# Kernel tuning notes

Measured on AMD Instinct MI355X. Metric: run time of the kernel, lower is better.

The kernel has to match this reference:

```python
import jax, jax.numpy as jnp
import numpy as np

# Model dims (see init_kwargs)
N_SITES = 1024
M_CAT = 2
TOKEN_DIM = 256
POS_DIM = 768
D_MODEL = TOKEN_DIM + POS_DIM  # 1024
D_FF = 4 * D_MODEL             # 4096
N_LAYERS = 4
N_HEADS = 16
HEAD_DIM = D_MODEL // N_HEADS  # 64
BATCH = 4
EPS = 1e-5


def setup_inputs() -> dict:
    key = jax.random.key(0)
    ks = jax.random.split(key, 8)
    s = 0.02  # init std, matches _init_weights
    L = N_LAYERS
    return {
        "x": jax.random.randint(ks[0], (BATCH, N_SITES), 0, M_CAT),
        "tok_emb": jax.random.normal(ks[1], (M_CAT, TOKEN_DIM), jnp.float32) * s,
        "pos_emb": jax.random.normal(ks[2], (N_SITES, POS_DIM), jnp.float32) * s,
        "w_qkv": jax.random.normal(ks[3], (L, 3 * D_MODEL, D_MODEL), jnp.float32) * s,
        "b_qkv": jnp.zeros((L, 3 * D_MODEL), jnp.float32),
        "ln1_g": jnp.ones((L, D_MODEL), jnp.float32),
        "ln1_b": jnp.zeros((L, D_MODEL), jnp.float32),
        "ln2_g": jnp.ones((L, D_MODEL), jnp.float32),
        "ln2_b": jnp.zeros((L, D_MODEL), jnp.float32),
        "ff_w1": jax.random.normal(ks[4], (L, D_FF, D_MODEL), jnp.float32) * s,
        "ff_b1": jnp.zeros((L, D_FF), jnp.float32),
        "ff_w2": jax.random.normal(ks[5], (L, D_MODEL, D_FF), jnp.float32) * s,
        "ff_b2": jnp.zeros((L, D_MODEL), jnp.float32),
        "out_w": jax.random.normal(ks[6], (M_CAT, D_MODEL), jnp.float32) * s,
        "out_b": jnp.zeros((M_CAT,), jnp.float32),
    }


def _layernorm(h, g, b):
    mu = jnp.mean(h, axis=-1, keepdims=True)
    var = jnp.mean(jnp.square(h - mu), axis=-1, keepdims=True)
    return (h - mu) * jax.lax.rsqrt(var + EPS) * g + b


def _forward(x, tok_emb, pos_emb, w_qkv, b_qkv, ln1_g, ln1_b, ln2_g, ln2_b,
             ff_w1, ff_b1, ff_w2, ff_b2, out_w, out_b):
    B, T = x.shape
    # shift right: prepend BOS token '1', drop last
    x_in = jnp.concatenate([jnp.ones((B, 1), dtype=x.dtype), x[:, :-1]], axis=1)
    h = jnp.concatenate([
        tok_emb[x_in],                                       # [B, T, TOKEN_DIM]
        jnp.broadcast_to(pos_emb[None, :T], (B, T, POS_DIM)),
    ], axis=-1)                                              # [B, T, D_MODEL]
    causal = jnp.tril(jnp.ones((T, T), dtype=bool))
    scale = 1.0 / np.sqrt(HEAD_DIM)
    for l in range(N_LAYERS):
        a = _layernorm(h, ln1_g[l], ln1_b[l])
        qkv = a @ w_qkv[l].T + b_qkv[l]                      # [B, T, 3*D]
        q, k, v = jnp.split(qkv, 3, axis=-1)
        q = q.reshape(B, T, N_HEADS, HEAD_DIM)
        k = k.reshape(B, T, N_HEADS, HEAD_DIM)
        v = v.reshape(B, T, N_HEADS, HEAD_DIM)
        scores = jnp.einsum('bthd,bshd->bhts', q, k) * scale
        scores = jnp.where(causal, scores, jnp.float32(-1e9))
        p = jax.nn.softmax(scores, axis=-1)
        attn = jnp.einsum('bhts,bshd->bthd', p, v).reshape(B, T, D_MODEL)
        h = h + attn                                          # residual (no out_proj, per decode loop)
        h = _layernorm(h, ln2_g[l], ln2_b[l])
        ff = jax.nn.gelu(h @ ff_w1[l].T + ff_b1[l]) @ ff_w2[l].T + ff_b2[l]
        h = h + ff
    logits = h @ out_w.T + out_b                              # [B, T, M]
    return jax.nn.log_softmax(logits, axis=-1)


def reference(x, tok_emb, pos_emb, w_qkv, b_qkv, ln1_g, ln1_b, ln2_g, ln2_b,
              ff_w1, ff_b1, ff_w2, ff_b2, out_w, out_b):
    return _forward(x, tok_emb, pos_emb, w_qkv, b_qkv, ln1_g, ln1_b, ln2_g, ln2_b,
                    ff_w1, ff_b1, ff_w2, ff_b2, out_w, out_b)
```

## Files before the change

### kernel.cpp

```cpp
#include <hip/hip_runtime.h>
#include <cstddef>
#include <cstdint>

#define BB   4
#define TS   1024
#define DM   1024
#define DFF  4096
#define NHD  16
#define HDM  64
#define NLY  4
#define TOKD 256
#define POSD 768

typedef __bf16 bf16_t;
typedef __bf16 bf16x4 __attribute__((ext_vector_type(4)));
typedef __bf16 bf16x8 __attribute__((ext_vector_type(8)));
typedef float  f32x4  __attribute__((ext_vector_type(4)));

#define GLOAD_LDS16(gp, lp)                                                  \
  __builtin_amdgcn_global_load_lds(                                          \
      (const __attribute__((address_space(1))) void*)(gp),                   \
      (__attribute__((address_space(3))) void*)(lp), 16, 0, 0)

__device__ __forceinline__ float gelu_f(float x) {
  float x3 = x * x * x;
  return 0.5f * x * (1.0f + tanhf(0.7978845608028654f * (x + 0.044715f * x3)));
}

__global__ __launch_bounds__(256) void k_embed(const int* __restrict__ x,
    const float* __restrict__ tok, const float* __restrict__ pos,
    bf16_t* __restrict__ h) {
  int idx = (blockIdx.x * 256 + threadIdx.x) * 4;
  int d  = idx & (DM - 1);
  int bt = idx >> 10;
  int t  = bt & (TS - 1);
  int b  = bt >> 10;
  float4 v;
  if (d < TOKD) {
    int tk = (t == 0) ? 1 : x[b * TS + t - 1];
    v = *(const float4*)(tok + tk * TOKD + d);
  } else {
    v = *(const float4*)(pos + (size_t)t * POSD + (d - TOKD));
  }
  bf16x4 o = { (bf16_t)v.x, (bf16_t)v.y, (bf16_t)v.z, (bf16_t)v.w };
  *(bf16x4*)(h + idx) = o;
}

__global__ __launch_bounds__(256) void k_ln(const bf16_t* __restrict__ in,
    const float* __restrict__ g, const float* __restrict__ bta,
    bf16_t* __restrict__ out1, bf16_t* __restrict__ out2) {
  int row  = blockIdx.x * 4 + (threadIdx.x >> 6);
  int lane = threadIdx.x & 63;
  const bf16_t* p = in + (size_t)row * DM + lane * 16;
  bf16x8 v0 = *(const bf16x8*)p;
  bf16x8 v1 = *(const bf16x8*)(p + 8);
  float vals[16];
  float s = 0.f, s2 = 0.f;
#pragma unroll
  for (int i = 0; i < 8; i++) { vals[i] = (float)v0[i]; vals[8 + i] = (float)v1[i]; }
#pragma unroll
  for (int i = 0; i < 16; i++) { s += vals[i]; s2 += vals[i] * vals[i]; }
#pragma unroll
  for (int off = 32; off; off >>= 1) {
    s  += __shfl_xor(s, off);
    s2 += __shfl_xor(s2, off);
  }
  float mu  = s * (1.f / DM);
  float var = s2 * (1.f / DM) - mu * mu;
  float rs  = rsqrtf(var + 1e-5f);
  bf16x8 o0, o1;
#pragma unroll
  for (int i = 0; i < 16; i++) {
    int d = lane * 16 + i;
    float v = (vals[i] - mu) * rs * g[d] + bta[d];
    if (i < 8) o0[i] = (bf16_t)v; else o1[i - 8] = (bf16_t)v;
  }
  size_t off = (size_t)row * DM + lane * 16;
  if (out1) { *(bf16x8*)(out1 + off) = o0; *(bf16x8*)(out1 + off + 8) = o1; }
  if (out2) { *(bf16x8*)(out2 + off) = o0; *(bf16x8*)(out2 + off + 8) = o1; }
}

template <bool GELU, bool ACC>
__global__ __launch_bounds__(256) void k_gemm(
    const bf16_t* __restrict__ A, const float* __restrict__ B,
    const float* __restrict__ bias, bf16_t* __restrict__ C,
    int M, int N, int K, int ldb) {
  __shared__ __align__(16) bf16_t As[128 * 32];
  __shared__ __align__(16) bf16_t Bs[128 * 32];
  const int tid  = threadIdx.x;
  const int wave = tid >> 6, lane = tid & 63;
  const int m0 = blockIdx.y * 128, n0 = blockIdx.x * 128;
  const int wm = (wave >> 1) * 64, wn = (wave & 1) * 64;
  f32x4 acc[4][4];
#pragma unroll
  for (int i = 0; i < 4; i++)
#pragma unroll
    for (int j = 0; j < 4; j++) acc[i][j] = {0.f, 0.f, 0.f, 0.f};

  const int srow = wave * 16 + (lane >> 2);
  const int scol = (lane & 3) * 8;
  const bf16_t* Ag = A + (size_t)(m0 + srow) * K + scol;
  bf16_t* AsW = As + wave * 16 * 32;
  const int brow = tid >> 3;
  const int bcol = (tid & 7) * 4;
  const float* Bg = B + (size_t)(n0 + brow) * ldb + bcol;
  const int fr = lane & 15, fq = lane >> 4;

  for (int k0 = 0; k0 < K; k0 += 32) {
    __syncthreads();
    GLOAD_LDS16(Ag + k0, AsW);
    GLOAD_LDS16(Ag + (size_t)64 * K + k0, AsW + 64 * 32);
#pragma unroll
    for (int i = 0; i < 4; i++) {
      float4 v = *(const float4*)(Bg + (size_t)(i * 32) * ldb + k0);
      bf16x4 o = { (bf16_t)v.x, (bf16_t)v.y, (bf16_t)v.z, (bf16_t)v.w };
      *(bf16x4*)&Bs[(brow + i * 32) * 32 + bcol] = o;
    }
    __syncthreads();
    bf16x8 af[4], bfv[4];
#pragma unroll
    for (int i = 0; i < 4; i++)
      af[i] = *(const bf16x8*)&As[(wm + i * 16 + fr) * 32 + fq * 8];
#pragma unroll
    for (int j = 0; j < 4; j++)
      bfv[j] = *(const bf16x8*)&Bs[(wn + j * 16 + fr) * 32 + fq * 8];
#pragma unroll
    for (int i = 0; i < 4; i++)
#pragma unroll
      for (int j = 0; j < 4; j++)
        acc[i][j] = __builtin_amdgcn_mfma_f32_16x16x32_bf16(
            af[i], bfv[j], acc[i][j], 0, 0, 0);
  }
#pragma unroll
  for (int i = 0; i < 4; i++) {
#pragma unroll
    for (int j = 0; j < 4; j++) {
#pragma unroll
      for (int r = 0; r < 4; r++) {
        int m = m0 + wm + i * 16 + fq * 4 + r;
        int n = n0 + wn + j * 16 + fr;
        float v = acc[i][j][r];
        if (bias) v += bias[n];
        if (GELU) v = gelu_f(v);
        size_t off = (size_t)m * N + n;
        if (ACC) C[off] = (bf16_t)((float)C[off] + v);
        else     C[off] = (bf16_t)v;
      }
    }
  }
}

__global__ __launch_bounds__(256) void k_flash(const bf16_t* __restrict__ qkv,
                                               bf16_t* __restrict__ hres) {
  __shared__ __align__(16) bf16_t Qs[64 * 72];
  __shared__ __align__(16) bf16_t Ks[64 * 72];
  __shared__ __align__(16) bf16_t Vt[64 * 72];
  const int hh = blockIdx.x, qt = blockIdx.y, bz = blockIdx.z;
  const int tid = threadIdx.x;
  const int w = tid >> 6, lane = tid & 63;
  const int fr = lane & 15, fq = lane >> 4;
  const int sr = tid >> 2, seg = tid & 3;
  const bf16_t* base = qkv + (size_t)bz * TS * (3 * DM) + hh * HDM;
  bf16_t* Ps = Qs;

  {
    const bf16_t* qrow = base + (size_t)(qt * 64 + sr) * (3 * DM) + seg * 16;
    *(bf16x8*)&Qs[sr * 72 + seg * 16]     = *(const bf16x8*)qrow;
    *(bf16x8*)&Qs[sr * 72 + seg * 16 + 8] = *(const bf16x8*)(qrow + 8);
  }
  __syncthreads();
  bf16x8 aq[2];
  aq[0] = *(const bf16x8*)&Qs[(w * 16 + fr) * 72 + fq * 8];
  aq[1] = *(const bf16x8*)&Qs[(w * 16 + fr) * 72 + 32 + fq * 8];

  f32x4 o[4];
#pragma unroll
  for (int d = 0; d < 4; d++) o[d] = {0.f, 0.f, 0.f, 0.f};
  float mval[4] = {-1e30f, -1e30f, -1e30f, -1e30f};
  float lsum[4] = {0.f, 0.f, 0.f, 0.f};

  for (int st = 0; st <= qt; st++) {
    __syncthreads();
    {
      size_t rowoff = (size_t)(st * 64 + sr) * (3 * DM);
      const bf16_t* krow = base + rowoff + DM + seg * 16;
      *(bf16x8*)&Ks[sr * 72 + seg * 16]     = *(const bf16x8*)krow;
      *(bf16x8*)&Ks[sr * 72 + seg * 16 + 8] = *(const bf16x8*)(krow + 8);
      const bf16_t* vrow = base + rowoff + 2 * DM + seg * 16;
      bf16x8 v0 = *(const bf16x8*)vrow;
      bf16x8 v1 = *(const bf16x8*)(vrow + 8);
#pragma unroll
      for (int j = 0; j < 8; j++) Vt[(seg * 16 + j) * 72 + sr]     = v0[j];
#pragma unroll
      for (int j = 0; j < 8; j++) Vt[(seg * 16 + 8 + j) * 72 + sr] = v1[j];
    }
    __syncthreads();
    f32x4 sacc[4];
#pragma unroll
    for (int j = 0; j < 4; j++) sacc[j] = {0.f, 0.f, 0.f, 0.f};
#pragma unroll
    for (int j = 0; j < 4; j++)
#pragma unroll
      for (int hf = 0; hf < 2; hf++) {
        bf16x8 bk = *(const bf16x8*)&Ks[(j * 16 + fr) * 72 + hf * 32 + fq * 8];
        sacc[j] = __builtin_amdgcn_mfma_f32_16x16x32_bf16(aq[hf], bk, sacc[j],
                                                          0, 0, 0);
      }
#pragma unroll
    for (int j = 0; j < 4; j++)
#pragma unroll
      for (int r = 0; r < 4; r++) {
        float s = sacc[j][r] * 0.125f;
        if (st == qt && (j * 16 + fr) > (w * 16 + fq * 4 + r)) s = -1e30f;
        sacc[j][r] = s;
      }
    float corr[4];
#pragma unroll
    for (int r = 0; r < 4; r++) {
      float v = fmaxf(fmaxf(sacc[0][r], sacc[1][r]),
                      fmaxf(sacc[2][r], sacc[3][r]));
      v = fmaxf(v, __shfl_xor(v, 1));
      v = fmaxf(v, __shfl_xor(v, 2));
      v = fmaxf(v, __shfl_xor(v, 4));
      v = fmaxf(v, __shfl_xor(v, 8));
      float mn = fmaxf(mval[r], v);
      corr[r] = __expf(mval[r] - mn);
      mval[r] = mn;
      lsum[r] *= corr[r];
    }
#pragma unroll
    for (int d = 0; d < 4; d++)
#pragma unroll
      for (int r = 0; r < 4; r++) o[d][r] *= corr[r];
    float rsum[4] = {0.f, 0.f, 0.f, 0.f};
#pragma unroll
    for (int j = 0; j < 4; j++)
#pragma unroll
      for (int r = 0; r < 4; r++) {
        float p = __expf(sacc[j][r] - mval[r]);
        rsum[r] += p;
        Ps[(w * 16 + fq * 4 + r) * 72 + j * 16 + fr] = (bf16_t)p;
      }
#pragma unroll
    for (int r = 0; r < 4; r++) {
      float v = rsum[r];
      v += __shfl_xor(v, 1);
      v += __shfl_xor(v, 2);
      v += __shfl_xor(v, 4);
      v += __shfl_xor(v, 8);
      lsum[r] += v;
    }
    __syncthreads();
    bf16x8 ap[2];
    ap[0] = *(const bf16x8*)&Ps[(w * 16 + fr) * 72 + fq * 8];
    ap[1] = *(const bf16x8*)&Ps[(w * 16 + fr) * 72 + 32 + fq * 8];
#pragma unroll
    for (int d = 0; d < 4; d++)
#pragma unroll
      for (int hf = 0; hf < 2; hf++) {
        bf16x8 bv = *(const bf16x8*)&Vt[(d * 16 + fr) * 72 + hf * 32 + fq * 8];
        o[d] = __builtin_amdgcn_mfma_f32_16x16x32_bf16(ap[hf], bv, o[d],
                                                       0, 0, 0);
      }
  }
#pragma unroll
  for (int r = 0; r < 4; r++) {
    float inv = 1.0f / lsum[r];
    bf16_t* row = hres + (size_t)bz * TS * DM +
                  (size_t)(qt * 64 + w * 16 + fq * 4 + r) * DM + hh * HDM;
#pragma unroll
    for (int d = 0; d < 4; d++) {
      int c = d * 16 + fr;
      row[c] = (bf16_t)((float)row[c] + o[d][r] * inv);
    }
  }
}

__global__ __launch_bounds__(256) void k_logits(const bf16_t* __restrict__ h,
    const float* __restrict__ w, const float* __restrict__ bz,
    float* __restrict__ out) {
  int row  = blockIdx.x * 4 + (threadIdx.x >> 6);
  int lane = threadIdx.x & 63;
  const bf16_t* hp = h + (size_t)row * DM + lane * 16;
  bf16x8 a0 = *(const bf16x8*)hp;
  bf16x8 a1 = *(const bf16x8*)(hp + 8);
  float s0 = 0.f, s1 = 0.f;
#pragma unroll
  for (int i = 0; i < 16; i++) {
    float v = (float)(i < 8 ? a0[i] : a1[i - 8]);
    int d = lane * 16 + i;
    s0 += v * w[d];
    s1 += v * w[DM + d];
  }
#pragma unroll
  for (int off = 32; off; off >>= 1) {
    s0 += __shfl_xor(s0, off);
    s1 += __shfl_xor(s1, off);
  }
  if (lane == 0) {
    float z0 = s0 + bz[0], z1 = s1 + bz[1];
    float mx  = fmaxf(z0, z1);
    float lse = mx + logf(expf(z0 - mx) + expf(z1 - mx));
    out[row * 2]     = z0 - lse;
    out[row * 2 + 1] = z1 - lse;
  }
}

extern "C" void kernel_launch(void* const* d_in, const int* in_sizes, int n_in,
                              void* d_out, int out_size, void* d_ws, size_t ws_size,
                              hipStream_t stream) {
  const int*   x     = (const int*)d_in[0];
  const float* tokE  = (const float*)d_in[1];
  const float* posE  = (const float*)d_in[2];
  const float* w_qkv = (const float*)d_in[3];
  const float* b_qkv = (const float*)d_in[4];
  const float* ln1g  = (const float*)d_in[5];
  const float* ln1b  = (const float*)d_in[6];
  const float* ln2g  = (const float*)d_in[7];
  const float* ln2b  = (const float*)d_in[8];
  const float* fw1   = (const float*)d_in[9];
  const float* fb1   = (const float*)d_in[10];
  const float* fw2   = (const float*)d_in[11];
  const float* fb2   = (const float*)d_in[12];
  const float* outw  = (const float*)d_in[13];
  const float* outb  = (const float*)d_in[14];
  float* out = (float*)d_out;

  const size_t NT = (size_t)BB * TS;
  const size_t MB = 1024 * 1024;
  bf16_t* h_bf = (bf16_t*)d_ws;
  char*   S    = (char*)d_ws + 8 * MB;
  bf16_t* a_bf   = (bf16_t*)S;
  bf16_t* qkv_bf = (bf16_t*)(S + 4 * MB);
  bf16_t* a2_bf  = (bf16_t*)S;
  bf16_t* f1_bf  = (bf16_t*)(S + 8 * MB);

  k_embed<<<(NT * DM) / 1024, 256, 0, stream>>>(x, tokE, posE, h_bf);
  for (int l = 0; l < NLY; l++) {
    for (int g = 0; g < 2; g++) {
      bf16_t* hg = h_bf + (size_t)g * 2 * TS * DM;
      k_ln<<<2 * TS / 4, 256, 0, stream>>>(hg, ln1g + l * DM, ln1b + l * DM,
                                           a_bf, nullptr);
      k_gemm<false, false><<<dim3(3 * DM / 128, 2 * TS / 128), 256, 0, stream>>>(
          a_bf, w_qkv + (size_t)l * 3 * DM * DM, b_qkv + l * 3 * DM, qkv_bf,
          2 * TS, 3 * DM, DM, DM);
      k_flash<<<dim3(NHD, TS / 64, 2), 256, 0, stream>>>(qkv_bf, hg);
    }
    k_ln<<<NT / 4, 256, 0, stream>>>(h_bf, ln2g + l * DM, ln2b + l * DM,
                                     h_bf, a2_bf);
    for (int s = 0; s < 2; s++) {
      k_gemm<true, false><<<dim3(2048 / 128, NT / 128), 256, 0, stream>>>(
          a2_bf, fw1 + (size_t)l * DFF * DM + (size_t)s * 2048 * DM,
          fb1 + l * DFF + s * 2048, f1_bf, NT, 2048, DM, DM);
      k_gemm<false, true><<<dim3(DM / 128, NT / 128), 256, 0, stream>>>(
          f1_bf, fw2 + (size_t)l * DM * DFF + s * 2048,
          s == 0 ? fb2 + l * DM : nullptr, h_bf, NT, DM, 2048, DFF);
    }
  }
  k_logits<<<NT / 4, 256, 0, stream>>>(h_bf, outw, outb, out);
}
```

Measured before the change: 2.217 ms.

## Double-buffer GEMM LDS tiles to overlap global loads with MFMA compute

Splits the A and B shared-memory tiles into two ping-pong buffers. The next K-tile's global-to-LDS A loads and the B register loads are issued before the current tile's MFMAs run, and the converted B values are written to LDS afterwards. This cuts the loop to one barrier per iteration and hides load latency behind compute. In exchange it doubles LDS use, which may lower occupancy, and keeps extra B values live in registers.

```diff
diff --git a/kernel.cpp b/kernel.cpp
--- a/kernel.cpp
+++ b/kernel.cpp
@@ -85,8 +85,8 @@
     const bf16_t* __restrict__ A, const float* __restrict__ B,
     const float* __restrict__ bias, bf16_t* __restrict__ C,
     int M, int N, int K, int ldb) {
-  __shared__ __align__(16) bf16_t As[128 * 32];
-  __shared__ __align__(16) bf16_t Bs[128 * 32];
+  __shared__ __align__(16) bf16_t As[2][128 * 32];
+  __shared__ __align__(16) bf16_t Bs[2][128 * 32];
   const int tid  = threadIdx.x;
   const int wave = tid >> 6, lane = tid & 63;
   const int m0 = blockIdx.y * 128, n0 = blockIdx.x * 128;
@@ -100,36 +100,61 @@
   const int srow = wave * 16 + (lane >> 2);
   const int scol = (lane & 3) * 8;
   const bf16_t* Ag = A + (size_t)(m0 + srow) * K + scol;
-  bf16_t* AsW = As + wave * 16 * 32;
+  const int aw0 = wave * 16 * 32;
+  const int aw1 = (64 + wave * 16) * 32;
   const int brow = tid >> 3;
   const int bcol = (tid & 7) * 4;
   const float* Bg = B + (size_t)(n0 + brow) * ldb + bcol;
   const int fr = lane & 15, fq = lane >> 4;
-
-  for (int k0 = 0; k0 < K; k0 += 32) {
-    __syncthreads();
-    GLOAD_LDS16(Ag + k0, AsW);
-    GLOAD_LDS16(Ag + (size_t)64 * K + k0, AsW + 64 * 32);
-#pragma unroll
-    for (int i = 0; i < 4; i++) {
-      float4 v = *(const float4*)(Bg + (size_t)(i * 32) * ldb + k0);
-      bf16x4 o = { (bf16_t)v.x, (bf16_t)v.y, (bf16_t)v.z, (bf16_t)v.w };
-      *(bf16x4*)&Bs[(brow + i * 32) * 32 + bcol] = o;
-    }
-    __syncthreads();
+  const int nt = K >> 5;
+
+  float4 breg[4];
+  GLOAD_LDS16(Ag, &As[0][aw0]);
+  GLOAD_LDS16(Ag + (size_t)64 * K, &As[0][aw1]);
+#pragma unroll
+  for (int i = 0; i < 4; i++)
+    breg[i] = *(const float4*)(Bg + (size_t)(i * 32) * ldb);
+#pragma unroll
+  for (int i = 0; i < 4; i++) {
+    bf16x4 o = { (bf16_t)breg[i].x, (bf16_t)breg[i].y,
+                 (bf16_t)breg[i].z, (bf16_t)breg[i].w };
+    *(bf16x4*)&Bs[0][(brow + i * 32) * 32 + bcol] = o;
+  }
+  __syncthreads();
+
+  int p = 0;
+  for (int t = 0; t < nt; t++, p ^= 1) {
+    const bool more = (t + 1 < nt);
+    const int k1 = (t + 1) << 5;
+    if (more) {
+      GLOAD_LDS16(Ag + k1, &As[p ^ 1][aw0]);
+      GLOAD_LDS16(Ag + (size_t)64 * K + k1, &As[p ^ 1][aw1]);
+#pragma unroll
+      for (int i = 0; i < 4; i++)
+        breg[i] = *(const float4*)(Bg + (size_t)(i * 32) * ldb + k1);
+    }
     bf16x8 af[4], bfv[4];
 #pragma unroll
     for (int i = 0; i < 4; i++)
-      af[i] = *(const bf16x8*)&As[(wm + i * 16 + fr) * 32 + fq * 8];
+      af[i] = *(const bf16x8*)&As[p][(wm + i * 16 + fr) * 32 + fq * 8];
 #pragma unroll
     for (int j = 0; j < 4; j++)
-      bfv[j] = *(const bf16x8*)&Bs[(wn + j * 16 + fr) * 32 + fq * 8];
+      bfv[j] = *(const bf16x8*)&Bs[p][(wn + j * 16 + fr) * 32 + fq * 8];
 #pragma unroll
     for (int i = 0; i < 4; i++)
 #pragma unroll
       for (int j = 0; j < 4; j++)
         acc[i][j] = __builtin_amdgcn_mfma_f32_16x16x32_bf16(
             af[i], bfv[j], acc[i][j], 0, 0, 0);
+    if (more) {
+#pragma unroll
+      for (int i = 0; i < 4; i++) {
+        bf16x4 o = { (bf16_t)breg[i].x, (bf16_t)breg[i].y,
+                     (bf16_t)breg[i].z, (bf16_t)breg[i].w };
+        *(bf16x4*)&Bs[p ^ 1][(brow + i * 32) * 32 + bcol] = o;
+      }
+    }
+    __syncthreads();
   }
 #pragma unroll
   for (int i = 0; i < 4; i++) {
```

Measured after the change: 2.076 ms. 1.07x faster.

## Triple-buffer GEMM LDS with register-staged B prefetch and templated N tile

Applied to the files above, without the earlier changes.

The GEMM's main loop becomes a software pipeline with three LDS stages. A tiles are issued two steps ahead through global_load_lds, and B tiles are prefetched into registers and written to LDS one step later. A single barrier per k-step replaces the two, and explicit vmcnt/lgkmcnt waits let global loads overlap MFMA compute. The N tile width is now a template parameter, with 64 used for the QKV and FF2 GEMMs to double the number of blocks. The cost is more LDS and register use, which may lower occupancy.

```diff
diff --git a/kernel.cpp b/kernel.cpp
--- a/kernel.cpp
+++ b/kernel.cpp
@@ -80,61 +80,104 @@
   if (out2) { *(bf16x8*)(out2 + off) = o0; *(bf16x8*)(out2 + off + 8) = o1; }
 }
 
-template <bool GELU, bool ACC>
+template <bool GELU, bool ACC, int TN>
 __global__ __launch_bounds__(256) void k_gemm(
     const bf16_t* __restrict__ A, const float* __restrict__ B,
     const float* __restrict__ bias, bf16_t* __restrict__ C,
     int M, int N, int K, int ldb) {
-  __shared__ __align__(16) bf16_t As[128 * 32];
-  __shared__ __align__(16) bf16_t Bs[128 * 32];
+  constexpr int NJ   = TN / 32;
+  constexpr int GOPS = 2 + NJ;
+  __shared__ __align__(16) bf16_t As[3][128 * 32];
+  __shared__ __align__(16) bf16_t Bs[3][TN * 32];
   const int tid  = threadIdx.x;
   const int wave = tid >> 6, lane = tid & 63;
-  const int m0 = blockIdx.y * 128, n0 = blockIdx.x * 128;
-  const int wm = (wave >> 1) * 64, wn = (wave & 1) * 64;
-  f32x4 acc[4][4];
+  const int m0 = blockIdx.y * 128, n0 = blockIdx.x * TN;
+  const int wm = (wave >> 1) * 64, wn = (wave & 1) * (TN / 2);
+  f32x4 acc[4][NJ];
 #pragma unroll
   for (int i = 0; i < 4; i++)
 #pragma unroll
-    for (int j = 0; j < 4; j++) acc[i][j] = {0.f, 0.f, 0.f, 0.f};
+    for (int j = 0; j < NJ; j++) acc[i][j] = {0.f, 0.f, 0.f, 0.f};
 
   const int srow = wave * 16 + (lane >> 2);
   const int scol = (lane & 3) * 8;
   const bf16_t* Ag = A + (size_t)(m0 + srow) * K + scol;
-  bf16_t* AsW = As + wave * 16 * 32;
+  const int aw0 = wave * 16 * 32;
+  const int aw1 = (64 + wave * 16) * 32;
   const int brow = tid >> 3;
   const int bcol = (tid & 7) * 4;
   const float* Bg = B + (size_t)(n0 + brow) * ldb + bcol;
   const int fr = lane & 15, fq = lane >> 4;
-
-  for (int k0 = 0; k0 < K; k0 += 32) {
-    __syncthreads();
-    GLOAD_LDS16(Ag + k0, AsW);
-    GLOAD_LDS16(Ag + (size_t)64 * K + k0, AsW + 64 * 32);
-#pragma unroll
-    for (int i = 0; i < 4; i++) {
-      float4 v = *(const float4*)(Bg + (size_t)(i * 32) * ldb + k0);
-      bf16x4 o = { (bf16_t)v.x, (bf16_t)v.y, (bf16_t)v.z, (bf16_t)v.w };
-      *(bf16x4*)&Bs[(brow + i * 32) * 32 + bcol] = o;
-    }
-    __syncthreads();
-    bf16x8 af[4], bfv[4];
-#pragma unroll
-    for (int i = 0; i < 4; i++)
-      af[i] = *(const bf16x8*)&As[(wm + i * 16 + fr) * 32 + fq * 8];
-#pragma unroll
-    for (int j = 0; j < 4; j++)
-      bfv[j] = *(const bf16x8*)&Bs[(wn + j * 16 + fr) * 32 + fq * 8];
-#pragma unroll
-    for (int i = 0; i < 4; i++)
-#pragma unroll
-      for (int j = 0; j < 4; j++)
-        acc[i][j] = __builtin_amdgcn_mfma_f32_16x16x32_bf16(
-            af[i], bfv[j], acc[i][j], 0, 0, 0);
-  }
+  const int nt = K >> 5;
+
+  float4 br0[NJ], br1[NJ];
+
+#define ISSUE_A(g) do { const int _k = (g) << 5; const int _b = (g) % 3;     \
+    GLOAD_LDS16(Ag + _k, &As[_b][aw0]);                                      \
+    GLOAD_LDS16(Ag + (size_t)64 * K + _k, &As[_b][aw1]); } while (0)
+#define LOAD_B(g, br) do { const int _k = (g) << 5;                          \
+    _Pragma("unroll")                                                        \
+    for (int _i = 0; _i < NJ; _i++)                                          \
+      br[_i] = *(const float4*)(Bg + (size_t)(_i * 32) * ldb + _k); } while (0)
+#define WRITE_B(g, br) do { const int _b = (g) % 3;                          \
+    _Pragma("unroll")                                                        \
+    for (int _i = 0; _i < NJ; _i++) {                                        \
+      bf16x4 _o = { (bf16_t)br[_i].x, (bf16_t)br[_i].y,                      \
+                    (bf16_t)br[_i].z, (bf16_t)br[_i].w };                    \
+      *(bf16x4*)&Bs[_b][(brow + _i * 32) * 32 + bcol] = _o; } } while (0)
+#define COMPUTE(g) do { const int _b = (g) % 3;                              \
+    bf16x8 _af[4], _bf[NJ];                                                  \
+    _Pragma("unroll")                                                        \
+    for (int _i = 0; _i < 4; _i++)                                           \
+      _af[_i] = *(const bf16x8*)&As[_b][(wm + _i * 16 + fr) * 32 + fq * 8];  \
+    _Pragma("unroll")                                                        \
+    for (int _j = 0; _j < NJ; _j++)                                          \
+      _bf[_j] = *(const bf16x8*)&Bs[_b][(wn + _j * 16 + fr) * 32 + fq * 8];  \
+    _Pragma("unroll")                                                        \
+    for (int _i = 0; _i < 4; _i++)                                           \
+      _Pragma("unroll")                                                      \
+      for (int _j = 0; _j < NJ; _j++)                                        \
+        acc[_i][_j] = __builtin_amdgcn_mfma_f32_16x16x32_bf16(               \
+            _af[_i], _bf[_j], acc[_i][_j], 0, 0, 0); } while (0)
+#define WAITV(n) asm volatile("s_waitcnt vmcnt(%0)" :: "n"(n) : "memory")
+#define KBAR() do { asm volatile("s_waitcnt lgkmcnt(0)" ::: "memory");       \
+                    __builtin_amdgcn_s_barrier(); } while (0)
+
+  ISSUE_A(0); LOAD_B(0, br0);
+  ISSUE_A(1); LOAD_B(1, br1);
+  WAITV(GOPS);
+  WRITE_B(0, br0);
+  KBAR();
+
+  for (int t = 0; t < nt - 2; t += 2) {
+    ISSUE_A(t + 2); LOAD_B(t + 2, br0);
+    WAITV(GOPS);
+    WRITE_B(t + 1, br1);
+    COMPUTE(t);
+    KBAR();
+    ISSUE_A(t + 3); LOAD_B(t + 3, br1);
+    WAITV(GOPS);
+    WRITE_B(t + 2, br0);
+    COMPUTE(t + 1);
+    KBAR();
+  }
+  WAITV(0);
+  WRITE_B(nt - 1, br1);
+  COMPUTE(nt - 2);
+  KBAR();
+  COMPUTE(nt - 1);
+
+#undef ISSUE_A
+#undef LOAD_B
+#undef WRITE_B
+#undef COMPUTE
+#undef WAITV
+#undef KBAR
+
 #pragma unroll
   for (int i = 0; i < 4; i++) {
 #pragma unroll
-    for (int j = 0; j < 4; j++) {
+    for (int j = 0; j < NJ; j++) {
 #pragma unroll
       for (int r = 0; r < 4; r++) {
         int m = m0 + wm + i * 16 + fq * 4 + r;
@@ -341,7 +384,7 @@
       bf16_t* hg = h_bf + (size_t)g * 2 * TS * DM;
       k_ln<<<2 * TS / 4, 256, 0, stream>>>(hg, ln1g + l * DM, ln1b + l * DM,
                                            a_bf, nullptr);
-      k_gemm<false, false><<<dim3(3 * DM / 128, 2 * TS / 128), 256, 0, stream>>>(
+      k_gemm<false, false, 64><<<dim3(3 * DM / 64, 2 * TS / 128), 256, 0, stream>>>(
           a_bf, w_qkv + (size_t)l * 3 * DM * DM, b_qkv + l * 3 * DM, qkv_bf,
           2 * TS, 3 * DM, DM, DM);
       k_flash<<<dim3(NHD, TS / 64, 2), 256, 0, stream>>>(qkv_bf, hg);
@@ -349,10 +392,10 @@
     k_ln<<<NT / 4, 256, 0, stream>>>(h_bf, ln2g + l * DM, ln2b + l * DM,
                                      h_bf, a2_bf);
     for (int s = 0; s < 2; s++) {
-      k_gemm<true, false><<<dim3(2048 / 128, NT / 128), 256, 0, stream>>>(
+      k_gemm<true, false, 128><<<dim3(2048 / 128, NT / 128), 256, 0, stream>>>(
           a2_bf, fw1 + (size_t)l * DFF * DM + (size_t)s * 2048 * DM,
           fb1 + l * DFF + s * 2048, f1_bf, NT, 2048, DM, DM);
-      k_gemm<false, true><<<dim3(DM / 128, NT / 128), 256, 0, stream>>>(
+      k_gemm<false, true, 64><<<dim3(DM / 64, NT / 128), 256, 0, stream>>>(
           f1_bf, fw2 + (size_t)l * DM * DFF + s * 2048,
           s == 0 ? fb2 + l * DM : nullptr, h_bf, NT, DM, 2048, DFF);
     }
```

Result: faster. 1.995 ms (-10.0%).
